# Kernel tuning notes

Measured on AMD Instinct MI355X. Metric: run time of the kernel, lower is better.

The kernel has to match this reference:

```python
import jax, jax.numpy as jnp
import numpy as np

N, E, G = 50000, 500000, 64
IN_F, H_F, HEADS, OUT_F = 128, 64, 4, 326000
NEG_SLOPE = 0.2


def _gat_layer(h, W, a_src, a_dst, b, src, dst):
    # h: [N, H_F]; W: [H_F, HEADS*H_F]; a_src/a_dst: [HEADS, H_F]; b: [H_F]
    x = (h @ W).reshape(N, HEADS, H_F)                      # per-head transform
    ls = jnp.einsum('nhc,hc->nh', x, a_src)                  # [N, HEADS]
    ld = jnp.einsum('nhc,hc->nh', x, a_dst)
    e = jax.nn.leaky_relu(ls[src] + ld[dst], NEG_SLOPE)      # [E', HEADS] edge logits
    m = jax.ops.segment_max(e, dst, num_segments=N)          # segment-softmax (stable)
    m = jnp.where(jnp.isfinite(m), m, 0.0)
    ex = jnp.exp(e - m[dst])
    denom = jax.ops.segment_sum(ex, dst, num_segments=N)
    alpha = ex / (denom[dst] + 1e-16)                        # [E', HEADS]
    out = jax.ops.segment_sum(x[src] * alpha[:, :, None], dst, num_segments=N)  # [N,HEADS,H_F]
    return out.mean(axis=1) + b                              # concat=False -> head mean + bias


def setup_inputs() -> dict:
    key = jax.random.key(0)
    ks = jax.random.split(key, 24)
    inp = {
        'x': jax.random.normal(ks[0], (N, IN_F), dtype=jnp.float32),
        'edge_index': jax.random.randint(ks[1], (2, E), 0, N, dtype=jnp.int32),
        'edge_attr': jax.random.normal(ks[2], (E, 16), dtype=jnp.float32),
        'batch': jnp.sort(jax.random.randint(ks[3], (N,), 0, G, dtype=jnp.int32)),
        'W_emb': jax.random.normal(ks[4], (IN_F, H_F), dtype=jnp.float32) * 0.05,
        'b_emb': jnp.zeros((H_F,), dtype=jnp.float32),
        'W_fc': jax.random.normal(ks[5], (H_F, OUT_F), dtype=jnp.float32) * 0.05,
        'b_fc': jnp.zeros((OUT_F,), dtype=jnp.float32),
    }
    for l in range(3):
        inp[f'W{l+1}'] = jax.random.normal(ks[6 + 4 * l], (H_F, HEADS * H_F), dtype=jnp.float32) * 0.05
        inp[f'a_src{l+1}'] = jax.random.normal(ks[7 + 4 * l], (HEADS, H_F), dtype=jnp.float32) * 0.1
        inp[f'a_dst{l+1}'] = jax.random.normal(ks[8 + 4 * l], (HEADS, H_F), dtype=jnp.float32) * 0.1
        inp[f'b{l+1}'] = jnp.zeros((H_F,), dtype=jnp.float32)
    return inp


def reference(x, edge_index, edge_attr, batch, W_emb, b_emb,
              W1, a_src1, a_dst1, b1, W2, a_src2, a_dst2, b2,
              W3, a_src3, a_dst3, b3, W_fc, b_fc):
    # add self loops (PyG GATConv default)
    loop = jnp.arange(N, dtype=edge_index.dtype)
    src = jnp.concatenate([edge_index[0], loop])
    dst = jnp.concatenate([edge_index[1], loop])

    h = x @ W_emb + b_emb
    for (W, a_s, a_d, b) in ((W1, a_src1, a_dst1, b1), (W2, a_src2, a_dst2, b2), (W3, a_src3, a_dst3, b3)):
        h = jax.nn.relu(_gat_layer(h, W, a_s, a_d, b, src, dst))

    # global mean pool over graphs
    sums = jax.ops.segment_sum(h, batch, num_segments=G)
    cnt = jax.ops.segment_sum(jnp.ones((N,), h.dtype), batch, num_segments=G)
    pooled = sums / jnp.maximum(cnt, 1.0)[:, None]
    # dropout is identity in eval mode
    return pooled @ W_fc + b_fc
```

## Files before the change

kernel.cpp:

```cpp
#include <hip/hip_runtime.h>

#define NN 50000
#define EE 500000
#define GG 64
#define IN_F 128
#define H_F 64
#define HEADS 4
#define OUT_F 326000
#define NEG 0.2f
#define SCAN_B 256
#define NBLK ((NN + SCAN_B - 1) / SCAN_B)

__global__ __launch_bounds__(256) void k_emb(const float* __restrict__ x,
                                             const float* __restrict__ Wemb,
                                             const float* __restrict__ bemb,
                                             float* __restrict__ h0) {
    __shared__ float wlds[IN_F * H_F];
    int t = threadIdx.x;
#pragma unroll
    for (int i = 0; i < (IN_F * H_F) / (4 * 256); ++i)
        ((float4*)wlds)[t + 256 * i] = ((const float4*)Wemb)[t + 256 * i];
    __syncthreads();

    int c = t & 63, sub = t >> 6;
    int n0 = __builtin_amdgcn_readfirstlane(blockIdx.x * 32 + sub * 8);
    float bv = bemb[c];

    if (n0 + 8 <= NN) {
        const float4* xr = (const float4*)(x + (size_t)n0 * IN_F);
        float acc[8] = {0.f, 0.f, 0.f, 0.f, 0.f, 0.f, 0.f, 0.f};
        for (int k4 = 0; k4 < IN_F / 4; ++k4) {
            float w0 = wlds[(4 * k4 + 0) * H_F + c];
            float w1 = wlds[(4 * k4 + 1) * H_F + c];
            float w2 = wlds[(4 * k4 + 2) * H_F + c];
            float w3 = wlds[(4 * k4 + 3) * H_F + c];
#pragma unroll
            for (int j = 0; j < 8; ++j) {
                float4 xv = xr[j * (IN_F / 4) + k4];
                acc[j] = fmaf(xv.x, w0,
                         fmaf(xv.y, w1,
                         fmaf(xv.z, w2,
                         fmaf(xv.w, w3, acc[j]))));
            }
        }
#pragma unroll
        for (int j = 0; j < 8; ++j)
            h0[(size_t)(n0 + j) * H_F + c] = acc[j] + bv;
    } else {
        for (int j = 0; j < 8; ++j) {
            int n = n0 + j;
            if (n >= NN) break;
            const float* xrow = x + (size_t)n * IN_F;
            float a = 0.f;
            for (int k = 0; k < IN_F; ++k) a += xrow[k] * wlds[k * H_F + c];
            h0[(size_t)n * H_F + c] = a + bv;
        }
    }
}

__global__ __launch_bounds__(256) void k_gemm_layer(const float* __restrict__ h,
                                                    const float* __restrict__ W,
                                                    const float* __restrict__ a_src,
                                                    const float* __restrict__ a_dst,
                                                    float* __restrict__ xbuf,
                                                    float* __restrict__ ls,
                                                    float* __restrict__ ld) {
    __shared__ float wlds[H_F * 128];
    int t = threadIdx.x;
    int hp = blockIdx.x & 1;
    int nbase = (blockIdx.x >> 1) * 32;
    {
        const float4* W4 = (const float4*)W;
        float4* wl4 = (float4*)wlds;
#pragma unroll
        for (int i = 0; i < 8; ++i) {
            int flat = t + 256 * i;
            int k = flat >> 5;
            int off = flat & 31;
            wl4[flat] = W4[k * 64 + hp * 32 + off];
        }
    }
    int lane = t & 63;
    int hd2 = (t >> 6) & 1;
    int q = t >> 7;
    int hd = hp * 2 + hd2;
    float asv = a_src[hd * 64 + lane];
    float adv = a_dst[hd * 64 + lane];
    __syncthreads();

    const float* wcol = wlds + hd2 * 64 + lane;
    for (int g = 0; g < 2; ++g) {
        int n0 = __builtin_amdgcn_readfirstlane(nbase + q * 16 + g * 8);
        if (n0 >= NN) break;
        const float4* hr = (const float4*)(h + (size_t)n0 * H_F);
        float acc[8] = {0.f, 0.f, 0.f, 0.f, 0.f, 0.f, 0.f, 0.f};
        for (int k4 = 0; k4 < H_F / 4; ++k4) {
            float w0 = wcol[(4 * k4 + 0) * 128];
            float w1 = wcol[(4 * k4 + 1) * 128];
            float w2 = wcol[(4 * k4 + 2) * 128];
            float w3 = wcol[(4 * k4 + 3) * 128];
#pragma unroll
            for (int j = 0; j < 8; ++j) {
                float4 hv = hr[j * (H_F / 4) + k4];
                acc[j] = fmaf(hv.x, w0,
                         fmaf(hv.y, w1,
                         fmaf(hv.z, w2,
                         fmaf(hv.w, w3, acc[j]))));
            }
        }
#pragma unroll
        for (int j = 0; j < 8; ++j) {
            int n = n0 + j;
            xbuf[(size_t)n * (HEADS * H_F) + lane * 4 + hd] = acc[j];
            float vs = acc[j] * asv, vd = acc[j] * adv;
#pragma unroll
            for (int off = 32; off; off >>= 1) {
                vs += __shfl_xor(vs, off, 64);
                vd += __shfl_xor(vd, off, 64);
            }
            if (lane == 0) {
                ls[n * HEADS + hd] = vs;
                ld[n * HEADS + hd] = vd;
            }
        }
    }
}

__device__ __forceinline__ float lrelu_exp(float e) {
    e = (e > 0.f) ? e : NEG * e;
    return __expf(e);
}

__device__ __forceinline__ float4 lexp4(float4 s, float4 d) {
    float4 r;
    r.x = lrelu_exp(s.x + d.x);
    r.y = lrelu_exp(s.y + d.y);
    r.z = lrelu_exp(s.z + d.z);
    r.w = lrelu_exp(s.w + d.w);
    return r;
}

__global__ void k_count(const int* __restrict__ dst, int* __restrict__ cnt) {
    int i = blockIdx.x * blockDim.x + threadIdx.x;
    if (i >= EE + NN) return;
    int d = (i < EE) ? dst[i] : (i - EE);
    atomicAdd(&cnt[d], 1);
}

__global__ void k_scan1(const int* __restrict__ cnt, int* __restrict__ excl,
                        int* __restrict__ bsum) {
    __shared__ int lds[SCAN_B];
    int t = threadIdx.x, i = blockIdx.x * SCAN_B + t;
    int v = (i < NN) ? cnt[i] : 0;
    lds[t] = v;
    __syncthreads();
    for (int off = 1; off < SCAN_B; off <<= 1) {
        int add = (t >= off) ? lds[t - off] : 0;
        __syncthreads();
        lds[t] += add;
        __syncthreads();
    }
    if (i < NN) excl[i] = lds[t] - v;
    if (t == SCAN_B - 1) bsum[blockIdx.x] = lds[t];
}

__global__ void k_scan2(int* __restrict__ bsum) {
    __shared__ int lds[SCAN_B];
    int t = threadIdx.x;
    int v = (t < NBLK) ? bsum[t] : 0;
    lds[t] = v;
    __syncthreads();
    for (int off = 1; off < SCAN_B; off <<= 1) {
        int add = (t >= off) ? lds[t - off] : 0;
        __syncthreads();
        lds[t] += add;
        __syncthreads();
    }
    if (t < NBLK) bsum[t] = lds[t] - v;
}

__global__ void k_scan3(const int* __restrict__ excl, const int* __restrict__ bsum,
                        int* __restrict__ row, int* __restrict__ cursor) {
    int i = blockIdx.x * blockDim.x + threadIdx.x;
    if (i >= NN) return;
    int r = excl[i] + bsum[i / SCAN_B];
    row[i] = r;
    cursor[i] = r;
    if (i == 0) row[NN] = EE + NN;
}

__global__ void k_scatter(const int* __restrict__ src, const int* __restrict__ dst,
                          int* __restrict__ cursor, int* __restrict__ csr_src) {
    int i = blockIdx.x * blockDim.x + threadIdx.x;
    if (i >= EE + NN) return;
    int s, d;
    if (i < EE) { s = src[i]; d = dst[i]; } else { s = d = i - EE; }
    int pos = atomicAdd(&cursor[d], 1);
    csr_src[pos] = s;
}

__global__ __launch_bounds__(256) void k_aggr_csr(const int* __restrict__ row,
                                                  const int* __restrict__ csr_src,
                                                  const float4* __restrict__ ls4,
                                                  const float4* __restrict__ ld4,
                                                  const float4* __restrict__ xb4,
                                                  const float* __restrict__ bias,
                                                  float* __restrict__ hout) {
    int t = threadIdx.x;
    int lane = t & 63, wv = t >> 6;
    int dA = blockIdx.x * 8 + wv * 2;
    int dB = dA + 1;
    if (dA >= NN) return;
    int r0A = row[dA], r1A = row[dA + 1];
    int r0B = row[dB], r1B = row[dB + 1];
    float4 bldA = ld4[dA];
    float4 bldB = ld4[dB];
    float4 accA = {0.f, 0.f, 0.f, 0.f}, denA = {1e-16f, 1e-16f, 1e-16f, 1e-16f};
    float4 accB = {0.f, 0.f, 0.f, 0.f}, denB = {1e-16f, 1e-16f, 1e-16f, 1e-16f};

    int jA = r0A, jB = r0B;
    int sA = (jA < r1A) ? csr_src[jA] : 0;
    int sB = (jB < r1B) ? csr_src[jB] : 0;

    while (jA < r1A && jB < r1B) {
        int sa = __builtin_amdgcn_readfirstlane(sA);
        int sb = __builtin_amdgcn_readfirstlane(sB);
        float4 xa = xb4[(size_t)sa * H_F + lane];
        float4 xb = xb4[(size_t)sb * H_F + lane];
        float4 la = ls4[sa];
        float4 lb = ls4[sb];
        ++jA; if (jA < r1A) sA = csr_src[jA];
        ++jB; if (jB < r1B) sB = csr_src[jB];
        float4 ea = lexp4(la, bldA);
        float4 eb = lexp4(lb, bldB);
        denA.x += ea.x; denA.y += ea.y; denA.z += ea.z; denA.w += ea.w;
        denB.x += eb.x; denB.y += eb.y; denB.z += eb.z; denB.w += eb.w;
        accA.x = fmaf(ea.x, xa.x, accA.x);
        accA.y = fmaf(ea.y, xa.y, accA.y);
        accA.z = fmaf(ea.z, xa.z, accA.z);
        accA.w = fmaf(ea.w, xa.w, accA.w);
        accB.x = fmaf(eb.x, xb.x, accB.x);
        accB.y = fmaf(eb.y, xb.y, accB.y);
        accB.z = fmaf(eb.z, xb.z, accB.z);
        accB.w = fmaf(eb.w, xb.w, accB.w);
    }
    while (jA < r1A) {
        int sa = __builtin_amdgcn_readfirstlane(sA);
        float4 xa = xb4[(size_t)sa * H_F + lane];
        float4 la = ls4[sa];
        ++jA; if (jA < r1A) sA = csr_src[jA];
        float4 ea = lexp4(la, bldA);
        denA.x += ea.x; denA.y += ea.y; denA.z += ea.z; denA.w += ea.w;
        accA.x = fmaf(ea.x, xa.x, accA.x);
        accA.y = fmaf(ea.y, xa.y, accA.y);
        accA.z = fmaf(ea.z, xa.z, accA.z);
        accA.w = fmaf(ea.w, xa.w, accA.w);
    }
    while (jB < r1B) {
        int sb = __builtin_amdgcn_readfirstlane(sB);
        float4 xb = xb4[(size_t)sb * H_F + lane];
        float4 lb = ls4[sb];
        ++jB; if (jB < r1B) sB = csr_src[jB];
        float4 eb = lexp4(lb, bldB);
        denB.x += eb.x; denB.y += eb.y; denB.z += eb.z; denB.w += eb.w;
        accB.x = fmaf(eb.x, xb.x, accB.x);
        accB.y = fmaf(eb.y, xb.y, accB.y);
        accB.z = fmaf(eb.z, xb.z, accB.z);
        accB.w = fmaf(eb.w, xb.w, accB.w);
    }

    float bv = bias[lane];
    float resA = 0.25f * (accA.x / denA.x + accA.y / denA.y +
                          accA.z / denA.z + accA.w / denA.w);
    float resB = 0.25f * (accB.x / denB.x + accB.y / denB.y +
                          accB.z / denB.z + accB.w / denB.w);
    hout[(size_t)dA * H_F + lane] = fmaxf(resA + bv, 0.f);
    hout[(size_t)dB * H_F + lane] = fmaxf(resB + bv, 0.f);
}

__global__ void k_starts(const int* __restrict__ batch, int* __restrict__ starts) {
    int g = threadIdx.x;
    if (g > GG) return;
    int lo = 0, hi = NN;
    while (lo < hi) {
        int mid = (lo + hi) >> 1;
        if (batch[mid] < g) lo = mid + 1; else hi = mid;
    }
    starts[g] = lo;
}

__global__ void k_pool(const float* __restrict__ h, const int* __restrict__ starts,
                       float* __restrict__ pooledT) {
    int g = blockIdx.x;
    int s = starts[g], e = starts[g + 1];
    int t = threadIdx.x;
    int c = t & 63, j = t >> 6;
    float sum = 0.f;
    for (int n = s + j; n < e; n += 4) sum += h[(size_t)n * H_F + c];
    __shared__ float lds[256];
    lds[t] = sum;
    __syncthreads();
    if (j == 0) {
        float tot = lds[c] + lds[64 + c] + lds[128 + c] + lds[192 + c];
        int cnt = e - s;
        float inv = 1.0f / (float)(cnt > 0 ? cnt : 1);
        pooledT[c * GG + g] = tot * inv;
    }
}

__global__ __launch_bounds__(256) void k_fc(const float* __restrict__ pooledT,
                                            const float* __restrict__ Wfc,
                                            const float* __restrict__ bfc,
                                            float* __restrict__ out) {
    int o = blockIdx.x * blockDim.x + threadIdx.x;
    if (o >= OUT_F) return;
    float acc[GG];
#pragma unroll
    for (int g = 0; g < GG; ++g) acc[g] = 0.f;
    for (int c = 0; c < H_F; ++c) {
        float w = Wfc[(size_t)c * OUT_F + o];
        const float4* pr4 = (const float4*)(pooledT + c * GG);
#pragma unroll
        for (int g4 = 0; g4 < GG / 4; ++g4) {
            float4 p = pr4[g4];
            acc[4 * g4 + 0] = fmaf(p.x, w, acc[4 * g4 + 0]);
            acc[4 * g4 + 1] = fmaf(p.y, w, acc[4 * g4 + 1]);
            acc[4 * g4 + 2] = fmaf(p.z, w, acc[4 * g4 + 2]);
            acc[4 * g4 + 3] = fmaf(p.w, w, acc[4 * g4 + 3]);
        }
    }
    float bv = bfc[o];
    for (int g = 0; g < GG; ++g) out[(size_t)g * OUT_F + o] = acc[g] + bv;
}

extern "C" void kernel_launch(void* const* d_in, const int* in_sizes, int n_in,
                              void* d_out, int out_size, void* d_ws, size_t ws_size,
                              hipStream_t stream) {
    const float* x      = (const float*)d_in[0];
    const int*   eidx   = (const int*)d_in[1];
    const int*   batch  = (const int*)d_in[3];
    const float* W_emb  = (const float*)d_in[4];
    const float* b_emb  = (const float*)d_in[5];
    const float* W_fc   = (const float*)d_in[6];
    const float* b_fc   = (const float*)d_in[7];
    const float* Wl[3]   = {(const float*)d_in[8],  (const float*)d_in[12], (const float*)d_in[16]};
    const float* asl[3]  = {(const float*)d_in[9],  (const float*)d_in[13], (const float*)d_in[17]};
    const float* adl[3]  = {(const float*)d_in[10], (const float*)d_in[14], (const float*)d_in[18]};
    const float* bl[3]   = {(const float*)d_in[11], (const float*)d_in[15], (const float*)d_in[19]};

    const int* src = eidx;
    const int* dst = eidx + EE;

    float* xbuf    = (float*)d_ws;
    float* hA      = xbuf + (size_t)NN * 256;
    float* hB      = hA + (size_t)NN * 64;
    float* ls      = hB + (size_t)NN * 64;
    float* ldb     = ls + (size_t)NN * 4;
    float* pooledT = ldb + (size_t)NN * 4;
    int*   starts  = (int*)(pooledT + GG * GG);
    int*   cnt     = starts + 128;
    int*   excl    = cnt + NN;
    int*   bsum    = excl + NN;
    int*   row     = bsum + 256;
    int*   cursor  = row + NN + 4;
    int*   csr_src = cursor + NN;

    hipMemsetAsync(cnt, 0, (size_t)NN * sizeof(int), stream);
    k_count<<<(EE + NN + 255) / 256, 256, 0, stream>>>(dst, cnt);
    k_scan1<<<NBLK, SCAN_B, 0, stream>>>(cnt, excl, bsum);
    k_scan2<<<1, SCAN_B, 0, stream>>>(bsum);
    k_scan3<<<(NN + 255) / 256, 256, 0, stream>>>(excl, bsum, row, cursor);
    k_scatter<<<(EE + NN + 255) / 256, 256, 0, stream>>>(src, dst, cursor, csr_src);

    k_emb<<<(NN + 31) / 32, 256, 0, stream>>>(x, W_emb, b_emb, hA);

    float* hcur = hA;
    float* hnext = hB;
    for (int l = 0; l < 3; ++l) {
        k_gemm_layer<<<2 * ((NN + 31) / 32), 256, 0, stream>>>(hcur, Wl[l], asl[l], adl[l],
                                                               xbuf, ls, ldb);
        k_aggr_csr<<<NN / 8, 256, 0, stream>>>(row, csr_src,
                                               (const float4*)ls, (const float4*)ldb,
                                               (const float4*)xbuf, bl[l], hnext);
        float* tmp = hcur; hcur = hnext; hnext = tmp;
    }

    k_starts<<<1, 128, 0, stream>>>(batch, starts);
    k_pool<<<GG, 256, 0, stream>>>(hcur, starts, pooledT);
    k_fc<<<(OUT_F + 255) / 256, 256, 0, stream>>>(pooledT, W_fc, b_fc, (float*)d_out);
}
```

Before: 979.0 us.

## Merge scan kernels, fold group-start search into pool, widen per-layer GEMM block

Three-kernel CSR prefix scan is replaced by a single 1024-thread block that scans chunks of 49 counts serially and then writes row and cursor. The separate group-start search kernel is removed and each pool block does its own binary searches. The layer GEMM now uses 512-thread blocks covering all four heads per node, staging the full W in LDS so each h row is loaded once instead of twice. This cuts launches and redundant loads, but the single-block scan does uncoalesced serial reads per thread and the larger LDS footprint may reduce occupancy.

```diff
diff --git a/kernel.cpp b/kernel.cpp
--- a/kernel.cpp
+++ b/kernel.cpp
@@ -8,8 +8,6 @@
 #define HEADS 4
 #define OUT_F 326000
 #define NEG 0.2f
-#define SCAN_B 256
-#define NBLK ((NN + SCAN_B - 1) / SCAN_B)
 
 __global__ __launch_bounds__(256) void k_emb(const float* __restrict__ x,
                                              const float* __restrict__ Wemb,
@@ -58,47 +56,38 @@
     }
 }
 
-__global__ __launch_bounds__(256) void k_gemm_layer(const float* __restrict__ h,
+__global__ __launch_bounds__(512) void k_gemm_layer(const float* __restrict__ h,
                                                     const float* __restrict__ W,
                                                     const float* __restrict__ a_src,
                                                     const float* __restrict__ a_dst,
                                                     float* __restrict__ xbuf,
                                                     float* __restrict__ ls,
                                                     float* __restrict__ ld) {
-    __shared__ float wlds[H_F * 128];
-    int t = threadIdx.x;
-    int hp = blockIdx.x & 1;
-    int nbase = (blockIdx.x >> 1) * 32;
+    __shared__ float wlds[H_F * 256];
+    int t = threadIdx.x;
     {
         const float4* W4 = (const float4*)W;
         float4* wl4 = (float4*)wlds;
 #pragma unroll
-        for (int i = 0; i < 8; ++i) {
-            int flat = t + 256 * i;
-            int k = flat >> 5;
-            int off = flat & 31;
-            wl4[flat] = W4[k * 64 + hp * 32 + off];
-        }
-    }
-    int lane = t & 63;
-    int hd2 = (t >> 6) & 1;
-    int q = t >> 7;
-    int hd = hp * 2 + hd2;
-    float asv = a_src[hd * 64 + lane];
-    float adv = a_dst[hd * 64 + lane];
+        for (int i = 0; i < 8; ++i)
+            wl4[t + 512 * i] = W4[t + 512 * i];
+    }
+    int tc = t & 255, grp = t >> 8;
+    int lane = tc & 63, hd = tc >> 6;
+    float asv = a_src[tc], adv = a_dst[tc];
     __syncthreads();
 
-    const float* wcol = wlds + hd2 * 64 + lane;
-    for (int g = 0; g < 2; ++g) {
-        int n0 = __builtin_amdgcn_readfirstlane(nbase + q * 16 + g * 8);
+    int base = blockIdx.x * 64 + grp * 32;
+    for (int g = 0; g < 4; ++g) {
+        int n0 = __builtin_amdgcn_readfirstlane(base + g * 8);
         if (n0 >= NN) break;
         const float4* hr = (const float4*)(h + (size_t)n0 * H_F);
         float acc[8] = {0.f, 0.f, 0.f, 0.f, 0.f, 0.f, 0.f, 0.f};
         for (int k4 = 0; k4 < H_F / 4; ++k4) {
-            float w0 = wcol[(4 * k4 + 0) * 128];
-            float w1 = wcol[(4 * k4 + 1) * 128];
-            float w2 = wcol[(4 * k4 + 2) * 128];
-            float w3 = wcol[(4 * k4 + 3) * 128];
+            float w0 = wlds[(4 * k4 + 0) * 256 + tc];
+            float w1 = wlds[(4 * k4 + 1) * 256 + tc];
+            float w2 = wlds[(4 * k4 + 2) * 256 + tc];
+            float w3 = wlds[(4 * k4 + 3) * 256 + tc];
 #pragma unroll
             for (int j = 0; j < 8; ++j) {
                 float4 hv = hr[j * (H_F / 4) + k4];
@@ -147,46 +136,31 @@
     atomicAdd(&cnt[d], 1);
 }
 
-__global__ void k_scan1(const int* __restrict__ cnt, int* __restrict__ excl,
-                        int* __restrict__ bsum) {
-    __shared__ int lds[SCAN_B];
-    int t = threadIdx.x, i = blockIdx.x * SCAN_B + t;
-    int v = (i < NN) ? cnt[i] : 0;
-    lds[t] = v;
+#define CHUNK 49
+__global__ __launch_bounds__(1024) void k_scan_one(const int* __restrict__ cnt,
+                                                   int* __restrict__ row,
+                                                   int* __restrict__ cursor) {
+    __shared__ int lds[1024];
+    int t = threadIdx.x;
+    int c0 = t * CHUNK;
+    int c1 = c0 + CHUNK; if (c1 > NN) c1 = NN;
+    int s = 0;
+    for (int i = c0; i < c1; ++i) s += cnt[i];
+    lds[t] = s;
     __syncthreads();
-    for (int off = 1; off < SCAN_B; off <<= 1) {
+    for (int off = 1; off < 1024; off <<= 1) {
         int add = (t >= off) ? lds[t - off] : 0;
         __syncthreads();
         lds[t] += add;
         __syncthreads();
     }
-    if (i < NN) excl[i] = lds[t] - v;
-    if (t == SCAN_B - 1) bsum[blockIdx.x] = lds[t];
-}
-
-__global__ void k_scan2(int* __restrict__ bsum) {
-    __shared__ int lds[SCAN_B];
-    int t = threadIdx.x;
-    int v = (t < NBLK) ? bsum[t] : 0;
-    lds[t] = v;
-    __syncthreads();
-    for (int off = 1; off < SCAN_B; off <<= 1) {
-        int add = (t >= off) ? lds[t - off] : 0;
-        __syncthreads();
-        lds[t] += add;
-        __syncthreads();
-    }
-    if (t < NBLK) bsum[t] = lds[t] - v;
-}
-
-__global__ void k_scan3(const int* __restrict__ excl, const int* __restrict__ bsum,
-                        int* __restrict__ row, int* __restrict__ cursor) {
-    int i = blockIdx.x * blockDim.x + threadIdx.x;
-    if (i >= NN) return;
-    int r = excl[i] + bsum[i / SCAN_B];
-    row[i] = r;
-    cursor[i] = r;
-    if (i == 0) row[NN] = EE + NN;
+    int run = (t > 0) ? lds[t - 1] : 0;
+    for (int i = c0; i < c1; ++i) {
+        row[i] = run;
+        cursor[i] = run;
+        run += cnt[i];
+    }
+    if (t == 0) row[NN] = EE + NN;
 }
 
 __global__ void k_scatter(const int* __restrict__ src, const int* __restrict__ dst,
@@ -278,21 +252,19 @@
     hout[(size_t)dB * H_F + lane] = fmaxf(resB + bv, 0.f);
 }
 
-__global__ void k_starts(const int* __restrict__ batch, int* __restrict__ starts) {
-    int g = threadIdx.x;
-    if (g > GG) return;
-    int lo = 0, hi = NN;
-    while (lo < hi) {
-        int mid = (lo + hi) >> 1;
-        if (batch[mid] < g) lo = mid + 1; else hi = mid;
-    }
-    starts[g] = lo;
-}
-
-__global__ void k_pool(const float* __restrict__ h, const int* __restrict__ starts,
+__global__ void k_pool(const float* __restrict__ h, const int* __restrict__ batch,
                        float* __restrict__ pooledT) {
     int g = blockIdx.x;
-    int s = starts[g], e = starts[g + 1];
+    int s, e;
+    {
+        int lo = 0, hi = NN;
+        while (lo < hi) { int mid = (lo + hi) >> 1; if (batch[mid] < g) lo = mid + 1; else hi = mid; }
+        s = lo;
+        lo = 0; hi = NN;
+        int g1 = g + 1;
+        while (lo < hi) { int mid = (lo + hi) >> 1; if (batch[mid] < g1) lo = mid + 1; else hi = mid; }
+        e = lo;
+    }
     int t = threadIdx.x;
     int c = t & 63, j = t >> 6;
     float sum = 0.f;
@@ -357,19 +329,14 @@
     float* ls      = hB + (size_t)NN * 64;
     float* ldb     = ls + (size_t)NN * 4;
     float* pooledT = ldb + (size_t)NN * 4;
-    int*   starts  = (int*)(pooledT + GG * GG);
-    int*   cnt     = starts + 128;
-    int*   excl    = cnt + NN;
-    int*   bsum    = excl + NN;
-    int*   row     = bsum + 256;
+    int*   cnt     = (int*)(pooledT + GG * GG);
+    int*   row     = cnt + NN;
     int*   cursor  = row + NN + 4;
     int*   csr_src = cursor + NN;
 
     hipMemsetAsync(cnt, 0, (size_t)NN * sizeof(int), stream);
     k_count<<<(EE + NN + 255) / 256, 256, 0, stream>>>(dst, cnt);
-    k_scan1<<<NBLK, SCAN_B, 0, stream>>>(cnt, excl, bsum);
-    k_scan2<<<1, SCAN_B, 0, stream>>>(bsum);
-    k_scan3<<<(NN + 255) / 256, 256, 0, stream>>>(excl, bsum, row, cursor);
+    k_scan_one<<<1, 1024, 0, stream>>>(cnt, row, cursor);
     k_scatter<<<(EE + NN + 255) / 256, 256, 0, stream>>>(src, dst, cursor, csr_src);
 
     k_emb<<<(NN + 31) / 32, 256, 0, stream>>>(x, W_emb, b_emb, hA);
@@ -377,15 +344,14 @@
     float* hcur = hA;
     float* hnext = hB;
     for (int l = 0; l < 3; ++l) {
-        k_gemm_layer<<<2 * ((NN + 31) / 32), 256, 0, stream>>>(hcur, Wl[l], asl[l], adl[l],
-                                                               xbuf, ls, ldb);
+        k_gemm_layer<<<(NN + 63) / 64, 512, 0, stream>>>(hcur, Wl[l], asl[l], adl[l],
+                                                         xbuf, ls, ldb);
         k_aggr_csr<<<NN / 8, 256, 0, stream>>>(row, csr_src,
                                                (const float4*)ls, (const float4*)ldb,
                                                (const float4*)xbuf, bl[l], hnext);
         float* tmp = hcur; hcur = hnext; hnext = tmp;
     }
 
-    k_starts<<<1, 128, 0, stream>>>(batch, starts);
-    k_pool<<<GG, 256, 0, stream>>>(hcur, starts, pooledT);
+    k_pool<<<GG, 256, 0, stream>>>(hcur, batch, pooledT);
     k_fc<<<(OUT_F + 255) / 256, 256, 0, stream>>>(pooledT, W_fc, b_fc, (float*)d_out);
 }
```

New measurement: 1.134 ms. +15.8%, slower.
